# Performance work log

Measured on AMD Instinct MI355X. Metric: run time of the kernel, lower is better.

The kernel has to match this reference:

```python
import jax, jax.numpy as jnp
import numpy as np

N_LINKS = 20000
N_PATHS = 100000
PLEN = 8          # fixed path length -> max_len in scatter_nd
DL = 32           # link_state_dim
DP = 32           # path_state_dim
RU = 256          # readout_units
T = 8             # message passing iterations


def _gru(x, h, W, U, bi, bh):
    # Keras GRUCell (reset_after=True): gates order [z, r, h]
    gi = x @ W + bi
    gh = h @ U + bh
    iz, ir, ih = jnp.split(gi, 3, axis=-1)
    hz, hr, hh = jnp.split(gh, 3, axis=-1)
    z = jax.nn.sigmoid(iz + hz)
    r = jax.nn.sigmoid(ir + hr)
    cand = jnp.tanh(ih + r * hh)
    return z * h + (1.0 - z) * cand


def setup_inputs() -> dict:
    key = jax.random.key(0)
    ks = jax.random.split(key, 24)
    s = 0.1
    traffic = jax.random.uniform(ks[0], (N_PATHS,), dtype=jnp.float32)
    packets = jax.random.uniform(ks[1], (N_PATHS,), dtype=jnp.float32)
    EqLambda = jax.random.uniform(ks[2], (N_PATHS,), dtype=jnp.float32)
    AvgPktSize = jax.random.uniform(ks[3], (N_PATHS,), dtype=jnp.float32)
    capacity = jax.random.uniform(ks[4], (N_LINKS,), dtype=jnp.float32) + 0.1
    queueSizes = jax.random.uniform(ks[5], (N_LINKS,), dtype=jnp.float32) + 0.1
    link_to_path = jax.random.randint(ks[6], (N_PATHS * PLEN,), 0, N_LINKS, dtype=jnp.int32)
    path_ids = jnp.repeat(jnp.arange(N_PATHS, dtype=jnp.int32), PLEN)
    sequence_path = jnp.tile(jnp.arange(PLEN, dtype=jnp.int32), N_PATHS)
    path_to_link = path_ids       # same (path,link) incidence, link-centric view
    sequence_links = link_to_path
    return {
        'traffic': traffic, 'packets': packets, 'EqLambda': EqLambda,
        'AvgPktSize': AvgPktSize, 'capacity': capacity, 'queueSizes': queueSizes,
        'link_to_path': link_to_path, 'path_ids': path_ids,
        'sequence_path': sequence_path, 'path_to_link': path_to_link,
        'sequence_links': sequence_links, 'n_links': N_LINKS, 'n_paths': N_PATHS,
        'Wp': jax.random.normal(ks[7], (DL, 3 * DP), dtype=jnp.float32) * s,
        'Up': jax.random.normal(ks[8], (DP, 3 * DP), dtype=jnp.float32) * s,
        'bip': jnp.zeros((3 * DP,), jnp.float32),
        'bhp': jnp.zeros((3 * DP,), jnp.float32),
        'Wl': jax.random.normal(ks[9], (DP, 3 * DL), dtype=jnp.float32) * s,
        'Ul': jax.random.normal(ks[10], (DL, 3 * DL), dtype=jnp.float32) * s,
        'bil': jnp.zeros((3 * DL,), jnp.float32),
        'bhl': jnp.zeros((3 * DL,), jnp.float32),
        'W1': jax.random.normal(ks[11], (DL, RU), dtype=jnp.float32) * s,
        'b1': jnp.zeros((RU,), jnp.float32),
        'W2': jax.random.normal(ks[12], (RU, RU), dtype=jnp.float32) * s,
        'b2': jnp.zeros((RU,), jnp.float32),
        'W3': jax.random.normal(ks[13], (RU, 1), dtype=jnp.float32) * s,
        'b3': jnp.zeros((1,), jnp.float32),
    }


def reference(traffic, packets, EqLambda, AvgPktSize, capacity, queueSizes,
              link_to_path, path_ids, sequence_path, path_to_link, sequence_links,
              n_links, n_paths,
              Wp, Up, bip, bhp, Wl, Ul, bil, bhl, W1, b1, W2, b2, W3, b3):
    link_state = jnp.concatenate(
        [capacity[:, None], queueSizes[:, None], jnp.zeros((n_links, DL - 2), jnp.float32)], axis=1)
    path_state = jnp.concatenate(
        [traffic[:, None], packets[:, None], EqLambda[:, None], AvgPktSize[:, None],
         jnp.zeros((n_paths, DP - 4), jnp.float32)], axis=1)

    for _ in range(T):
        # gather link states along each path, scatter into padded [P, L, DL]
        link_gather = link_state[link_to_path]
        link_inputs = jnp.zeros((n_paths, PLEN, DL), jnp.float32).at[path_ids, sequence_path].set(link_gather)
        mask = jnp.any(link_inputs != 0.0, axis=-1)  # keras Masking: all-zero steps skipped

        def step(h, xm):
            x, m = xm
            h_new = _gru(x, h, Wp, Up, bip, bhp)
            return jnp.where(m[:, None], h_new, h), None

        path_state, _ = jax.lax.scan(step, path_state,
                                     (jnp.swapaxes(link_inputs, 0, 1), mask.T))
        # aggregate path states onto links
        path_gather = path_state[path_to_link]
        path_sum = jax.ops.segment_sum(path_gather, sequence_links, num_segments=n_links)
        link_state = _gru(path_sum, link_state, Wl, Ul, bil, bhl)

    r = jax.nn.relu(link_state @ W1 + b1)
    r = jax.nn.relu(r @ W2 + b2)  # dropout is identity at inference
    return r @ W3 + b3  # [n_links, 1]
```

## Files before the change

kernel.cpp:

```cpp
#include <hip/hip_runtime.h>

#define DPDIM 32
#define GCOLS 96
#define PLEN 8
#define T_ITERS 8
#define RUNITS 256

__device__ __forceinline__ float fast_sigmoid(float a) {
    return __builtin_amdgcn_rcpf(1.0f + __expf(-a));
}
__device__ __forceinline__ float fast_tanh(float a) {
    return 1.0f - 2.0f * __builtin_amdgcn_rcpf(1.0f + __expf(2.0f * a));
}

#define ACC4F(A, s, V) \
    A.x = fmaf((s), (V).x, A.x); A.y = fmaf((s), (V).y, A.y); \
    A.z = fmaf((s), (V).z, A.z); A.w = fmaf((s), (V).w, A.w);

__global__ __launch_bounds__(256) void init_kernel(
    const float* __restrict__ traffic, const float* __restrict__ packets,
    const float* __restrict__ eqlam, const float* __restrict__ avgpkt,
    const float* __restrict__ capacity, const float* __restrict__ queues,
    float* __restrict__ path_state, float* __restrict__ link_state,
    int n_paths, int n_links)
{
    int i = blockIdx.x * 256 + threadIdx.x;
    if (i < n_paths) {
        float4* row = (float4*)(path_state + (size_t)i * DPDIM);
        row[0] = make_float4(traffic[i], packets[i], eqlam[i], avgpkt[i]);
        float4 z = make_float4(0.f, 0.f, 0.f, 0.f);
        #pragma unroll
        for (int k = 1; k < 8; ++k) row[k] = z;
    }
    if (i < n_links) {
        float4* row = (float4*)(link_state + (size_t)i * DPDIM);
        row[0] = make_float4(capacity[i], queues[i], 0.f, 0.f);
        float4 z = make_float4(0.f, 0.f, 0.f, 0.f);
        #pragma unroll
        for (int k = 1; k < 8; ++k) row[k] = z;
    }
}

__global__ __launch_bounds__(256) void transpose_w_kernel(
    const float* __restrict__ W, float* __restrict__ T)
{
    int i = blockIdx.x * 256 + threadIdx.x;
    if (i >= 8*32*12) return;
    int idx = i % 12;
    int k   = (i / 12) % 32;
    int jb  = i / (12*32);
    int gate = idx >> 2, c = idx & 3;
    T[i] = W[k*GCOLS + gate*32 + jb*4 + c];
}

__global__ __launch_bounds__(256) void zero_counts_kernel(int* __restrict__ counts, int n) {
    int i = blockIdx.x * 256 + threadIdx.x;
    if (i < n) counts[i] = 0;
}
__global__ __launch_bounds__(256) void hist_kernel(
    const int* __restrict__ link_to_path, int* __restrict__ counts, int n) {
    int i = blockIdx.x * 256 + threadIdx.x;
    if (i < n) atomicAdd(&counts[link_to_path[i]], 1);
}
__global__ __launch_bounds__(1024) void scan_kernel(
    const int* __restrict__ counts, int* __restrict__ offsets,
    int* __restrict__ cursor, int n)
{
    __shared__ int s[1024];
    int t = threadIdx.x;
    int chunk = (n + 1023) >> 10;
    int lo = t * chunk;
    int hi = lo + chunk; if (hi > n) hi = n;
    int local = 0;
    for (int i = lo; i < hi; ++i) local += counts[i];
    s[t] = local;
    __syncthreads();
    for (int d = 1; d < 1024; d <<= 1) {
        int v = (t >= d) ? s[t - d] : 0;
        __syncthreads();
        s[t] += v;
        __syncthreads();
    }
    int base = (t > 0) ? s[t - 1] : 0;
    for (int i = lo; i < hi; ++i) {
        offsets[i] = base; cursor[i] = base; base += counts[i];
    }
    if (t == 1023) offsets[n] = s[1023];
}
__global__ __launch_bounds__(256) void fill_kernel(
    const int* __restrict__ link_to_path, int* __restrict__ cursor,
    int* __restrict__ entries, int n) {
    int e = blockIdx.x * 256 + threadIdx.x;
    if (e < n) {
        int l = link_to_path[e];
        int pos = atomicAdd(&cursor[l], 1);
        entries[pos] = e >> 3;
    }
}

__global__ __launch_bounds__(256, 1) void gate_pre_kernel(
    const float* __restrict__ link_state,
    const float* __restrict__ WpT, const float* __restrict__ bip,
    const float* __restrict__ bhp,
    float* __restrict__ Gi, int* __restrict__ nzf, int n_links)
{
    int t = threadIdx.x;
    int pe = t & 63;
    int eps = __builtin_amdgcn_readfirstlane(t >> 6);
    int l = blockIdx.x * 64 + pe;
    bool act = l < n_links;
    int ll = act ? l : (n_links - 1);

    float x[DPDIM];
    bool nz = false;
    {
        const float4* row = (const float4*)(link_state + (size_t)ll * DPDIM);
        #pragma unroll
        for (int k4 = 0; k4 < 8; ++k4) {
            float4 v = row[k4];
            x[4*k4+0]=v.x; x[4*k4+1]=v.y; x[4*k4+2]=v.z; x[4*k4+3]=v.w;
            nz = nz || (v.x != 0.f) || (v.y != 0.f) || (v.z != 0.f) || (v.w != 0.f);
        }
    }
    float* G = Gi + (size_t)ll * GCOLS;
    int jb0 = eps*2;
    #pragma unroll 1
    for (int jj = 0; jj < 2; ++jj) {
        int jb = jb0 + jj;
        float4 az = {0,0,0,0}, ar = {0,0,0,0}, ah = {0,0,0,0};
        const float* w = WpT + jb*(32*12);
        #pragma unroll 4
        for (int k = 0; k < DPDIM; ++k) {
            float xk = x[k];
            const float4 wz = *(const float4*)(w);
            const float4 wr = *(const float4*)(w + 4);
            const float4 wh = *(const float4*)(w + 8);
            ACC4F(az, xk, wz); ACC4F(ar, xk, wr); ACC4F(ah, xk, wh);
            w += 12;
        }
        const float4 bz = *(const float4*)(bip + jb*4);
        const float4 br = *(const float4*)(bip + 32 + jb*4);
        const float4 bh = *(const float4*)(bip + 64 + jb*4);
        const float4 cz = *(const float4*)(bhp + jb*4);
        const float4 cr = *(const float4*)(bhp + 32 + jb*4);
        if (act) {
            *(float4*)(G + jb*4)      = make_float4(az.x+bz.x+cz.x, az.y+bz.y+cz.y,
                                                    az.z+bz.z+cz.z, az.w+bz.w+cz.w);
            *(float4*)(G + 32 + jb*4) = make_float4(ar.x+br.x+cr.x, ar.y+br.y+cr.y,
                                                    ar.z+br.z+cr.z, ar.w+br.w+cr.w);
            *(float4*)(G + 64 + jb*4) = make_float4(ah.x+bh.x, ah.y+bh.y,
                                                    ah.z+bh.z, ah.w+bh.w);
        }
    }
    if (act && eps == 0) nzf[l] = nz ? 1 : 0;
}

__global__ __launch_bounds__(256, 1) void path_kernel(
    const float* __restrict__ Gi, const int* __restrict__ nzf,
    float* __restrict__ path_state, const int* __restrict__ link_to_path,
    const float* __restrict__ UpT, const float* __restrict__ bhp, int n_paths)
{
    __shared__ float hbuf[2*DPDIM*64];
    int t = threadIdx.x;
    int pe = t & 63;
    int eps = __builtin_amdgcn_readfirstlane(t >> 6);
    int p = blockIdx.x * 64 + pe;
    bool act = p < n_paths;
    int pp = act ? p : (n_paths - 1);

    {
        const float4* row = (const float4*)(path_state + (size_t)pp * DPDIM + eps*8);
        float4 v0 = row[0], v1 = row[1];
        int c0 = eps*8;
        hbuf[(c0+0)*64 + pe] = v0.x; hbuf[(c0+1)*64 + pe] = v0.y;
        hbuf[(c0+2)*64 + pe] = v0.z; hbuf[(c0+3)*64 + pe] = v0.w;
        hbuf[(c0+4)*64 + pe] = v1.x; hbuf[(c0+5)*64 + pe] = v1.y;
        hbuf[(c0+6)*64 + pe] = v1.z; hbuf[(c0+7)*64 + pe] = v1.w;
    }
    __syncthreads();

    int cur = 0;
    int jb0 = eps*2;
    #pragma unroll 1
    for (int s = 0; s < PLEN; ++s) {
        int l = link_to_path[pp*PLEN + s];
        bool nz = act && (nzf[l] != 0);
        const float* G = Gi + (size_t)l * GCOLS;
        const float* hold = hbuf + cur*(DPDIM*64) + pe;
        float* hnew = hbuf + (cur^1)*(DPDIM*64) + pe;
        #pragma unroll 1
        for (int jj = 0; jj < 2; ++jj) {
            int jb = jb0 + jj;
            float4 az  = *(const float4*)(G + jb*4);
            float4 ar  = *(const float4*)(G + 32 + jb*4);
            float4 gih = *(const float4*)(G + 64 + jb*4);
            float4 ah  = *(const float4*)(bhp + 64 + jb*4);
            const float* w = UpT + jb*(32*12);
            #pragma unroll 4
            for (int k = 0; k < DPDIM; ++k) {
                float hk = hold[k*64];
                const float4 wz = *(const float4*)(w);
                const float4 wr = *(const float4*)(w + 4);
                const float4 wh = *(const float4*)(w + 8);
                ACC4F(az, hk, wz); ACC4F(ar, hk, wr); ACC4F(ah, hk, wh);
                w += 12;
            }
#define PWC(C, j) { \
            float zz = fast_sigmoid(az.C); \
            float rr = fast_sigmoid(ar.C); \
            float cc = fast_tanh(gih.C + rr * ah.C); \
            float ho = hold[(jb*4+j)*64]; \
            hnew[(jb*4+j)*64] = nz ? (cc + zz * (ho - cc)) : ho; }
            PWC(x, 0) PWC(y, 1) PWC(z, 2) PWC(w, 3)
#undef PWC
        }
        __syncthreads();
        cur ^= 1;
    }

    if (act) {
        const float* hf = hbuf + cur*(DPDIM*64) + pe;
        int c0 = eps*8;
        float4 a = make_float4(hf[(c0+0)*64], hf[(c0+1)*64],
                               hf[(c0+2)*64], hf[(c0+3)*64]);
        float4 b = make_float4(hf[(c0+4)*64], hf[(c0+5)*64],
                               hf[(c0+6)*64], hf[(c0+7)*64]);
        *(float4*)(path_state + (size_t)p * DPDIM + c0)     = a;
        *(float4*)(path_state + (size_t)p * DPDIM + c0 + 4) = b;
    }
}

__global__ __launch_bounds__(256) void seg_sum_kernel(
    const float* __restrict__ path_state, const int* __restrict__ offsets,
    const int* __restrict__ entries, float* __restrict__ path_sum, int n_links)
{
    int t = threadIdx.x;
    int d = t & 31, li = t >> 5;
    int l = blockIdx.x * 8 + li;
    if (l >= n_links) return;
    int beg = offsets[l], end = offsets[l+1];
    float a0 = 0.f, a1 = 0.f, a2 = 0.f, a3 = 0.f;
    int q = beg;
    for (; q + 3 < end; q += 4) {
        int p0 = entries[q], p1 = entries[q+1], p2 = entries[q+2], p3 = entries[q+3];
        a0 += path_state[(size_t)p0 * DPDIM + d];
        a1 += path_state[(size_t)p1 * DPDIM + d];
        a2 += path_state[(size_t)p2 * DPDIM + d];
        a3 += path_state[(size_t)p3 * DPDIM + d];
    }
    for (; q < end; ++q)
        a0 += path_state[(size_t)entries[q] * DPDIM + d];
    path_sum[(size_t)l * DPDIM + d] = (a0 + a1) + (a2 + a3);
}

__global__ __launch_bounds__(256, 1) void link_kernel(
    const float* __restrict__ path_sum, float* __restrict__ link_state,
    const float* __restrict__ WlT, const float* __restrict__ UlT,
    const float* __restrict__ bil, const float* __restrict__ bhl, int n_links)
{
    __shared__ float xbuf[DPDIM*64];
    __shared__ float hbuf[DPDIM*64];
    int t = threadIdx.x;
    int pe = t & 63;
    int eps = __builtin_amdgcn_readfirstlane(t >> 6);
    int l = blockIdx.x * 64 + pe;
    bool act = l < n_links;
    int ll = act ? l : (n_links - 1);
    int c0 = eps*8;
    {
        const float4* xr = (const float4*)(path_sum  + (size_t)ll * DPDIM + c0);
        const float4* hr = (const float4*)(link_state + (size_t)ll * DPDIM + c0);
        float4 x0 = xr[0], x1 = xr[1], h0 = hr[0], h1 = hr[1];
        xbuf[(c0+0)*64 + pe] = x0.x; xbuf[(c0+1)*64 + pe] = x0.y;
        xbuf[(c0+2)*64 + pe] = x0.z; xbuf[(c0+3)*64 + pe] = x0.w;
        xbuf[(c0+4)*64 + pe] = x1.x; xbuf[(c0+5)*64 + pe] = x1.y;
        xbuf[(c0+6)*64 + pe] = x1.z; xbuf[(c0+7)*64 + pe] = x1.w;
        hbuf[(c0+0)*64 + pe] = h0.x; hbuf[(c0+1)*64 + pe] = h0.y;
        hbuf[(c0+2)*64 + pe] = h0.z; hbuf[(c0+3)*64 + pe] = h0.w;
        hbuf[(c0+4)*64 + pe] = h1.x; hbuf[(c0+5)*64 + pe] = h1.y;
        hbuf[(c0+6)*64 + pe] = h1.z; hbuf[(c0+7)*64 + pe] = h1.w;
    }
    __syncthreads();

    int jb0 = eps*2;
    #pragma unroll 1
    for (int jj = 0; jj < 2; ++jj) {
        int jb = jb0 + jj;
        float4 az = {0,0,0,0}, ar = {0,0,0,0}, ai = {0,0,0,0}, ah = {0,0,0,0};
        const float* w = WlT + jb*(32*12);
        const float* u = UlT + jb*(32*12);
        #pragma unroll 4
        for (int k = 0; k < DPDIM; ++k) {
            float xk = xbuf[k*64 + pe];
            float hk = hbuf[k*64 + pe];
            const float4 wz = *(const float4*)(w);
            const float4 wr = *(const float4*)(w + 4);
            const float4 wh = *(const float4*)(w + 8);
            const float4 uz = *(const float4*)(u);
            const float4 ur = *(const float4*)(u + 4);
            const float4 uh = *(const float4*)(u + 8);
            ACC4F(az, xk, wz); ACC4F(az, hk, uz);
            ACC4F(ar, xk, wr); ACC4F(ar, hk, ur);
            ACC4F(ai, xk, wh);
            ACC4F(ah, hk, uh);
            w += 12; u += 12;
        }
        const float4 BZI = *(const float4*)(bil + jb*4);
        const float4 BRI = *(const float4*)(bil + 32 + jb*4);
        const float4 BHI = *(const float4*)(bil + 64 + jb*4);
        const float4 BZH = *(const float4*)(bhl + jb*4);
        const float4 BRH = *(const float4*)(bhl + 32 + jb*4);
        const float4 BHH = *(const float4*)(bhl + 64 + jb*4);
        float4 hv;
#define LWC(C, j, DST) { \
        float z = fast_sigmoid(az.C + BZI.C + BZH.C); \
        float r = fast_sigmoid(ar.C + BRI.C + BRH.C); \
        float c = fast_tanh(ai.C + BHI.C + r * (ah.C + BHH.C)); \
        float ho = hbuf[(jb*4+j)*64 + pe]; \
        DST = z*ho + (1.f - z)*c; }
        LWC(x, 0, hv.x) LWC(y, 1, hv.y) LWC(z, 2, hv.z) LWC(w, 3, hv.w)
#undef LWC
        if (act) *(float4*)(link_state + (size_t)ll * DPDIM + jb*4) = hv;
    }
}

__global__ __launch_bounds__(512, 1) void readout_kernel(
    const float* __restrict__ link_state,
    const float* __restrict__ W1, const float* __restrict__ b1,
    const float* __restrict__ W2, const float* __restrict__ b2,
    const float* __restrict__ W3, const float* __restrict__ b3,
    float* __restrict__ out, int n_links)
{
    __shared__ float s_m[64*257];
    __shared__ float s_part[8*64];
    int t = threadIdx.x;
    int u = t & 63;
    int g = __builtin_amdgcn_readfirstlane(t >> 6);
    int l = blockIdx.x * 64 + u;
    bool act = l < n_links;
    int ll = act ? l : (n_links - 1);

    float x[DPDIM];
    {
        const float4* row = (const float4*)(link_state + (size_t)ll * DPDIM);
        #pragma unroll
        for (int k4 = 0; k4 < 8; ++k4) {
            float4 v = row[k4];
            x[4*k4+0]=v.x; x[4*k4+1]=v.y; x[4*k4+2]=v.z; x[4*k4+3]=v.w;
        }
    }
    {
        const float* w1p = W1 + 32*g;
        const float* b1p = b1 + 32*g;
        float acc1[32];
        #pragma unroll
        for (int c = 0; c < 32; ++c) acc1[c] = b1p[c];
        #pragma unroll 2
        for (int k = 0; k < DPDIM; ++k) {
            float xk = x[k];
            #pragma unroll
            for (int c = 0; c < 32; ++c)
                acc1[c] = fmaf(xk, w1p[k*RUNITS + c], acc1[c]);
        }
        #pragma unroll
        for (int c = 0; c < 32; ++c)
            s_m[u*257 + 32*g + c] = fmaxf(acc1[c], 0.f);
    }
    __syncthreads();
    float acc[32];
    {
        const float* w2p = W2 + 32*g;
        const float* b2p = b2 + 32*g;
        #pragma unroll
        for (int c = 0; c < 32; ++c) acc[c] = b2p[c];
        const float* rrow = s_m + u*257;
        #pragma unroll 2
        for (int k = 0; k < RUNITS; ++k) {
            float rk = rrow[k];
            #pragma unroll
            for (int c = 0; c < 32; ++c)
                acc[c] = fmaf(rk, w2p[k*RUNITS + c], acc[c]);
        }
    }
    {
        const float* w3p = W3 + 32*g;
        float psum = 0.f;
        #pragma unroll
        for (int c = 0; c < 32; ++c)
            psum += fmaxf(acc[c], 0.f) * w3p[c];
        s_part[g*64 + u] = psum;
    }
    __syncthreads();
    if (t < 64 && act) {
        float ssum = b3[0];
        #pragma unroll
        for (int gg = 0; gg < 8; ++gg) ssum += s_part[gg*64 + u];
        out[l] = ssum;
    }
}

extern "C" void kernel_launch(void* const* d_in, const int* in_sizes, int n_in,
                              void* d_out, int out_size, void* d_ws, size_t ws_size,
                              hipStream_t stream)
{
    const float* traffic  = (const float*)d_in[0];
    const float* packets  = (const float*)d_in[1];
    const float* eqlam    = (const float*)d_in[2];
    const float* avgpkt   = (const float*)d_in[3];
    const float* capacity = (const float*)d_in[4];
    const float* queues   = (const float*)d_in[5];
    const int* link_to_path = (const int*)d_in[6];
    const float* Wp  = (const float*)d_in[13];
    const float* Up  = (const float*)d_in[14];
    const float* bip = (const float*)d_in[15];
    const float* bhp = (const float*)d_in[16];
    const float* Wl  = (const float*)d_in[17];
    const float* Ul  = (const float*)d_in[18];
    const float* bil = (const float*)d_in[19];
    const float* bhl = (const float*)d_in[20];
    const float* W1  = (const float*)d_in[21];
    const float* b1  = (const float*)d_in[22];
    const float* W2  = (const float*)d_in[23];
    const float* b2  = (const float*)d_in[24];
    const float* W3  = (const float*)d_in[25];
    const float* b3  = (const float*)d_in[26];
    const int n_paths = in_sizes[0];
    const int n_links = in_sizes[4];
    const int n_ent   = in_sizes[6];

    char* ws = (char*)d_ws;
    size_t off = 0;
    auto salloc = [&](size_t bytes) -> void* {
        void* p = ws + off;
        off += (bytes + 255) & ~size_t(255);
        return p;
    };
    float* path_state = (float*)salloc((size_t)n_paths * DPDIM * 4);
    float* link_state = (float*)salloc((size_t)n_links * DPDIM * 4);
    float* Gi         = (float*)salloc((size_t)n_links * GCOLS * 4);
    float* path_sum   = Gi;
    float* UpT   = (float*)salloc((size_t)8 * 32 * 12 * 4);
    float* WpT   = (float*)salloc((size_t)8 * 32 * 12 * 4);
    float* WlT   = (float*)salloc((size_t)8 * 32 * 12 * 4);
    float* UlT   = (float*)salloc((size_t)8 * 32 * 12 * 4);
    int* nzf     = (int*)salloc((size_t)n_links * 4);
    int* counts  = (int*)salloc((size_t)n_links * 4);
    int* offsets = (int*)salloc((size_t)(n_links + 1) * 4);
    int* cursor  = (int*)salloc((size_t)n_links * 4);
    int* entries = (int*)salloc((size_t)n_ent * 4);
    (void)ws_size; (void)n_in; (void)out_size;

    int gmax = ( (n_paths > n_links ? n_paths : n_links) + 255 ) / 256;
    zero_counts_kernel<<<(n_links + 255)/256, 256, 0, stream>>>(counts, n_links);
    init_kernel<<<gmax, 256, 0, stream>>>(traffic, packets, eqlam, avgpkt,
                                          capacity, queues, path_state, link_state,
                                          n_paths, n_links);
    transpose_w_kernel<<<(8*32*12 + 255)/256, 256, 0, stream>>>(Up, UpT);
    transpose_w_kernel<<<(8*32*12 + 255)/256, 256, 0, stream>>>(Wp, WpT);
    transpose_w_kernel<<<(8*32*12 + 255)/256, 256, 0, stream>>>(Wl, WlT);
    transpose_w_kernel<<<(8*32*12 + 255)/256, 256, 0, stream>>>(Ul, UlT);
    hist_kernel<<<(n_ent + 255)/256, 256, 0, stream>>>(link_to_path, counts, n_ent);
    scan_kernel<<<1, 1024, 0, stream>>>(counts, offsets, cursor, n_links);
    fill_kernel<<<(n_ent + 255)/256, 256, 0, stream>>>(link_to_path, cursor, entries, n_ent);

    int lgrid = (n_links + 63) / 64;
    for (int it = 0; it < T_ITERS; ++it) {
        gate_pre_kernel<<<lgrid, 256, 0, stream>>>(
            link_state, WpT, bip, bhp, Gi, nzf, n_links);
        path_kernel<<<(n_paths + 63)/64, 256, 0, stream>>>(
            Gi, nzf, path_state, link_to_path, UpT, bhp, n_paths);
        seg_sum_kernel<<<(n_links + 7)/8, 256, 0, stream>>>(
            path_state, offsets, entries, path_sum, n_links);
        link_kernel<<<lgrid, 256, 0, stream>>>(
            path_sum, link_state, WlT, UlT, bil, bhl, n_links);
    }
    readout_kernel<<<lgrid, 512, 0, stream>>>(
        link_state, W1, b1, W2, b2, W3, b3, (float*)d_out, n_links);
}
```

Before: 1.399 ms.

## Fuse segment-sum, link GRU and gate precompute; prefetch next link gates in path kernel

```diff
diff --git a/kernel.cpp b/kernel.cpp
--- a/kernel.cpp
+++ b/kernel.cpp
@@ -177,43 +177,86 @@
         hbuf[(c0+4)*64 + pe] = v1.x; hbuf[(c0+5)*64 + pe] = v1.y;
         hbuf[(c0+6)*64 + pe] = v1.z; hbuf[(c0+7)*64 + pe] = v1.w;
     }
+
+    const int jbA = eps*2, jbB = eps*2 + 1;
+    const float4 ahA0 = *(const float4*)(bhp + 64 + jbA*4);
+    const float4 ahB0 = *(const float4*)(bhp + 64 + jbB*4);
+    const float* wA0 = UpT + jbA*(32*12);
+    const float* wB0 = UpT + jbB*(32*12);
+
+    int l_s = link_to_path[pp*PLEN + 0];
+    int l_n = link_to_path[pp*PLEN + 1];
+    const float* G0 = Gi + (size_t)l_s * GCOLS;
+    float4 pazA = *(const float4*)(G0 + jbA*4);
+    float4 parA = *(const float4*)(G0 + 32 + jbA*4);
+    float4 pgihA= *(const float4*)(G0 + 64 + jbA*4);
+    float4 pazB = *(const float4*)(G0 + jbB*4);
+    float4 parB = *(const float4*)(G0 + 32 + jbB*4);
+    float4 pgihB= *(const float4*)(G0 + 64 + jbB*4);
+    int pnz = nzf[l_s];
+
     __syncthreads();
 
     int cur = 0;
-    int jb0 = eps*2;
     #pragma unroll 1
     for (int s = 0; s < PLEN; ++s) {
-        int l = link_to_path[pp*PLEN + s];
-        bool nz = act && (nzf[l] != 0);
-        const float* G = Gi + (size_t)l * GCOLS;
+        float4 azA = pazA, arA = parA, gihA = pgihA;
+        float4 azB = pazB, arB = parB, gihB = pgihB;
+        bool nz = act && (pnz != 0);
+        if (s < PLEN-1) {
+            const float* G1 = Gi + (size_t)l_n * GCOLS;
+            pazA = *(const float4*)(G1 + jbA*4);
+            parA = *(const float4*)(G1 + 32 + jbA*4);
+            pgihA= *(const float4*)(G1 + 64 + jbA*4);
+            pazB = *(const float4*)(G1 + jbB*4);
+            parB = *(const float4*)(G1 + 32 + jbB*4);
+            pgihB= *(const float4*)(G1 + 64 + jbB*4);
+            pnz = nzf[l_n];
+            if (s < PLEN-2) l_n = link_to_path[pp*PLEN + s + 2];
+        }
         const float* hold = hbuf + cur*(DPDIM*64) + pe;
         float* hnew = hbuf + (cur^1)*(DPDIM*64) + pe;
-        #pragma unroll 1
-        for (int jj = 0; jj < 2; ++jj) {
-            int jb = jb0 + jj;
-            float4 az  = *(const float4*)(G + jb*4);
-            float4 ar  = *(const float4*)(G + 32 + jb*4);
-            float4 gih = *(const float4*)(G + 64 + jb*4);
-            float4 ah  = *(const float4*)(bhp + 64 + jb*4);
-            const float* w = UpT + jb*(32*12);
+#define PWC1(C, j, az, ar, gih, ah, jb) { \
+        float zz = fast_sigmoid((az).C); \
+        float rr = fast_sigmoid((ar).C); \
+        float cc = fast_tanh((gih).C + rr * (ah).C); \
+        float ho = hold[((jb)*4+(j))*64]; \
+        hnew[((jb)*4+(j))*64] = nz ? (cc + zz * (ho - cc)) : ho; }
+        {
+            float4 ah = ahA0;
+            const float* w = wA0;
             #pragma unroll 4
             for (int k = 0; k < DPDIM; ++k) {
                 float hk = hold[k*64];
                 const float4 wz = *(const float4*)(w);
                 const float4 wr = *(const float4*)(w + 4);
                 const float4 wh = *(const float4*)(w + 8);
-                ACC4F(az, hk, wz); ACC4F(ar, hk, wr); ACC4F(ah, hk, wh);
+                ACC4F(azA, hk, wz); ACC4F(arA, hk, wr); ACC4F(ah, hk, wh);
                 w += 12;
             }
-#define PWC(C, j) { \
-            float zz = fast_sigmoid(az.C); \
-            float rr = fast_sigmoid(ar.C); \
-            float cc = fast_tanh(gih.C + rr * ah.C); \
-            float ho = hold[(jb*4+j)*64]; \
-            hnew[(jb*4+j)*64] = nz ? (cc + zz * (ho - cc)) : ho; }
-            PWC(x, 0) PWC(y, 1) PWC(z, 2) PWC(w, 3)
-#undef PWC
-        }
+            PWC1(x, 0, azA, arA, gihA, ah, jbA)
+            PWC1(y, 1, azA, arA, gihA, ah, jbA)
+            PWC1(z, 2, azA, arA, gihA, ah, jbA)
+            PWC1(w, 3, azA, arA, gihA, ah, jbA)
+        }
+        {
+            float4 ah = ahB0;
+            const float* w = wB0;
+            #pragma unroll 4
+            for (int k = 0; k < DPDIM; ++k) {
+                float hk = hold[k*64];
+                const float4 wz = *(const float4*)(w);
+                const float4 wr = *(const float4*)(w + 4);
+                const float4 wh = *(const float4*)(w + 8);
+                ACC4F(azB, hk, wz); ACC4F(arB, hk, wr); ACC4F(ah, hk, wh);
+                w += 12;
+            }
+            PWC1(x, 0, azB, arB, gihB, ah, jbB)
+            PWC1(y, 1, azB, arB, gihB, ah, jbB)
+            PWC1(z, 2, azB, arB, gihB, ah, jbB)
+            PWC1(w, 3, azB, arB, gihB, ah, jbB)
+        }
+#undef PWC1
         __syncthreads();
         cur ^= 1;
     }
@@ -230,55 +273,56 @@
     }
 }
 
-__global__ __launch_bounds__(256) void seg_sum_kernel(
+__global__ __launch_bounds__(256, 1) void link_update_kernel(
     const float* __restrict__ path_state, const int* __restrict__ offsets,
-    const int* __restrict__ entries, float* __restrict__ path_sum, int n_links)
-{
-    int t = threadIdx.x;
-    int d = t & 31, li = t >> 5;
-    int l = blockIdx.x * 8 + li;
-    if (l >= n_links) return;
-    int beg = offsets[l], end = offsets[l+1];
-    float a0 = 0.f, a1 = 0.f, a2 = 0.f, a3 = 0.f;
-    int q = beg;
-    for (; q + 3 < end; q += 4) {
-        int p0 = entries[q], p1 = entries[q+1], p2 = entries[q+2], p3 = entries[q+3];
-        a0 += path_state[(size_t)p0 * DPDIM + d];
-        a1 += path_state[(size_t)p1 * DPDIM + d];
-        a2 += path_state[(size_t)p2 * DPDIM + d];
-        a3 += path_state[(size_t)p3 * DPDIM + d];
-    }
-    for (; q < end; ++q)
-        a0 += path_state[(size_t)entries[q] * DPDIM + d];
-    path_sum[(size_t)l * DPDIM + d] = (a0 + a1) + (a2 + a3);
-}
-
-__global__ __launch_bounds__(256, 1) void link_kernel(
-    const float* __restrict__ path_sum, float* __restrict__ link_state,
+    const int* __restrict__ entries, float* __restrict__ link_state,
     const float* __restrict__ WlT, const float* __restrict__ UlT,
-    const float* __restrict__ bil, const float* __restrict__ bhl, int n_links)
+    const float* __restrict__ bil, const float* __restrict__ bhl,
+    const float* __restrict__ WpT, const float* __restrict__ bip,
+    const float* __restrict__ bhp,
+    float* __restrict__ Gi, int* __restrict__ nzf, int n_links)
 {
     __shared__ float xbuf[DPDIM*64];
     __shared__ float hbuf[DPDIM*64];
+    __shared__ float nbuf[DPDIM*64];
     int t = threadIdx.x;
     int pe = t & 63;
     int eps = __builtin_amdgcn_readfirstlane(t >> 6);
-    int l = blockIdx.x * 64 + pe;
+    int lb = blockIdx.x * 64;
+    int l = lb + pe;
     bool act = l < n_links;
     int ll = act ? l : (n_links - 1);
     int c0 = eps*8;
-    {
-        const float4* xr = (const float4*)(path_sum  + (size_t)ll * DPDIM + c0);
+
+    {
         const float4* hr = (const float4*)(link_state + (size_t)ll * DPDIM + c0);
-        float4 x0 = xr[0], x1 = xr[1], h0 = hr[0], h1 = hr[1];
-        xbuf[(c0+0)*64 + pe] = x0.x; xbuf[(c0+1)*64 + pe] = x0.y;
-        xbuf[(c0+2)*64 + pe] = x0.z; xbuf[(c0+3)*64 + pe] = x0.w;
-        xbuf[(c0+4)*64 + pe] = x1.x; xbuf[(c0+5)*64 + pe] = x1.y;
-        xbuf[(c0+6)*64 + pe] = x1.z; xbuf[(c0+7)*64 + pe] = x1.w;
+        float4 h0 = hr[0], h1 = hr[1];
         hbuf[(c0+0)*64 + pe] = h0.x; hbuf[(c0+1)*64 + pe] = h0.y;
         hbuf[(c0+2)*64 + pe] = h0.z; hbuf[(c0+3)*64 + pe] = h0.w;
         hbuf[(c0+4)*64 + pe] = h1.x; hbuf[(c0+5)*64 + pe] = h1.y;
         hbuf[(c0+6)*64 + pe] = h1.z; hbuf[(c0+7)*64 + pe] = h1.w;
+    }
+    {
+        int d = t & 31, li = t >> 5;
+        #pragma unroll 1
+        for (int lg = 0; lg < 8; ++lg) {
+            int ls = lb + lg*8 + li;
+            float a0 = 0.f, a1 = 0.f, a2 = 0.f, a3 = 0.f;
+            if (ls < n_links) {
+                int beg = offsets[ls], end = offsets[ls+1];
+                int q = beg;
+                for (; q + 3 < end; q += 4) {
+                    int p0 = entries[q], p1 = entries[q+1], p2 = entries[q+2], p3 = entries[q+3];
+                    a0 += path_state[(size_t)p0 * DPDIM + d];
+                    a1 += path_state[(size_t)p1 * DPDIM + d];
+                    a2 += path_state[(size_t)p2 * DPDIM + d];
+                    a3 += path_state[(size_t)p3 * DPDIM + d];
+                }
+                for (; q < end; ++q)
+                    a0 += path_state[(size_t)entries[q] * DPDIM + d];
+            }
+            xbuf[d*64 + lg*8 + li] = (a0 + a1) + (a2 + a3);
+        }
     }
     __syncthreads();
 
@@ -320,7 +364,49 @@
         DST = z*ho + (1.f - z)*c; }
         LWC(x, 0, hv.x) LWC(y, 1, hv.y) LWC(z, 2, hv.z) LWC(w, 3, hv.w)
 #undef LWC
+        nbuf[(jb*4+0)*64 + pe] = hv.x; nbuf[(jb*4+1)*64 + pe] = hv.y;
+        nbuf[(jb*4+2)*64 + pe] = hv.z; nbuf[(jb*4+3)*64 + pe] = hv.w;
         if (act) *(float4*)(link_state + (size_t)ll * DPDIM + jb*4) = hv;
+    }
+    __syncthreads();
+
+    {
+        float* G = Gi + (size_t)ll * GCOLS;
+        #pragma unroll 1
+        for (int jj = 0; jj < 2; ++jj) {
+            int jb = jb0 + jj;
+            float4 az = {0,0,0,0}, ar = {0,0,0,0}, ah = {0,0,0,0};
+            const float* w = WpT + jb*(32*12);
+            #pragma unroll 4
+            for (int k = 0; k < DPDIM; ++k) {
+                float xk = nbuf[k*64 + pe];
+                const float4 wz = *(const float4*)(w);
+                const float4 wr = *(const float4*)(w + 4);
+                const float4 wh = *(const float4*)(w + 8);
+                ACC4F(az, xk, wz); ACC4F(ar, xk, wr); ACC4F(ah, xk, wh);
+                w += 12;
+            }
+            const float4 bz = *(const float4*)(bip + jb*4);
+            const float4 br = *(const float4*)(bip + 32 + jb*4);
+            const float4 bh = *(const float4*)(bip + 64 + jb*4);
+            const float4 cz = *(const float4*)(bhp + jb*4);
+            const float4 cr = *(const float4*)(bhp + 32 + jb*4);
+            if (act) {
+                *(float4*)(G + jb*4)      = make_float4(az.x+bz.x+cz.x, az.y+bz.y+cz.y,
+                                                        az.z+bz.z+cz.z, az.w+bz.w+cz.w);
+                *(float4*)(G + 32 + jb*4) = make_float4(ar.x+br.x+cr.x, ar.y+br.y+cr.y,
+                                                        ar.z+br.z+cr.z, ar.w+br.w+cr.w);
+                *(float4*)(G + 64 + jb*4) = make_float4(ah.x+bh.x, ah.y+bh.y,
+                                                        ah.z+bh.z, ah.w+bh.w);
+            }
+        }
+        if (eps == 0) {
+            bool nz = false;
+            #pragma unroll 4
+            for (int k = 0; k < DPDIM; ++k)
+                nz = nz || (nbuf[k*64 + pe] != 0.f);
+            if (act) nzf[l] = nz ? 1 : 0;
+        }
     }
 }
 
@@ -438,7 +524,6 @@
     float* path_state = (float*)salloc((size_t)n_paths * DPDIM * 4);
     float* link_state = (float*)salloc((size_t)n_links * DPDIM * 4);
     float* Gi         = (float*)salloc((size_t)n_links * GCOLS * 4);
-    float* path_sum   = Gi;
     float* UpT   = (float*)salloc((size_t)8 * 32 * 12 * 4);
     float* WpT   = (float*)salloc((size_t)8 * 32 * 12 * 4);
     float* WlT   = (float*)salloc((size_t)8 * 32 * 12 * 4);
@@ -464,15 +549,14 @@
     fill_kernel<<<(n_ent + 255)/256, 256, 0, stream>>>(link_to_path, cursor, entries, n_ent);
 
     int lgrid = (n_links + 63) / 64;
+    gate_pre_kernel<<<lgrid, 256, 0, stream>>>(
+        link_state, WpT, bip, bhp, Gi, nzf, n_links);
     for (int it = 0; it < T_ITERS; ++it) {
-        gate_pre_kernel<<<lgrid, 256, 0, stream>>>(
-            link_state, WpT, bip, bhp, Gi, nzf, n_links);
         path_kernel<<<(n_paths + 63)/64, 256, 0, stream>>>(
             Gi, nzf, path_state, link_to_path, UpT, bhp, n_paths);
-        seg_sum_kernel<<<(n_links + 7)/8, 256, 0, stream>>>(
-            path_state, offsets, entries, path_sum, n_links);
-        link_kernel<<<lgrid, 256, 0, stream>>>(
-            path_sum, link_state, WlT, UlT, bil, bhl, n_links);
+        link_update_kernel<<<lgrid, 256, 0, stream>>>(
+            path_state, offsets, entries, link_state,
+            WlT, UlT, bil, bhl, WpT, bip, bhp, Gi, nzf, n_links);
     }
     readout_kernel<<<lgrid, 512, 0, stream>>>(
         link_state, W1, b1, W2, b2, W3, b3, (float*)d_out, n_links);
```

Result: slower. 1.604 ms (+14.7%).
